# Kernel optimization log

Measured on AMD Instinct MI355X. Metric: run time of the kernel, lower is better.

Reference implementation:

```python
import jax, jax.numpy as jnp
import numpy as np

NUM_HEADS = 32
NUM_KV_HEADS = 8
HEAD_DIM = 64
HIDDEN = 2048
EPS = 1e-05
ROPE_THETA = 1000000.0


def _rmsnorm(x, w):
    # x: [..., head_dim]
    var = jnp.mean(x * x, axis=-1, keepdims=True)
    return w * (x * jax.lax.rsqrt(var + EPS))


def _rope(q, k):
    # q,k: [B, h, T, d]
    T, d = q.shape[2], q.shape[3]
    inv_freq = 1.0 / (ROPE_THETA ** (jnp.arange(0, d, 2, dtype=jnp.float32) / d))
    t = jnp.arange(T, dtype=jnp.float32)
    freqs = jnp.outer(t, inv_freq)               # [T, d/2]
    emb = jnp.concatenate([freqs, freqs], -1)    # [T, d]
    cos = jnp.cos(emb)[None, None].astype(q.dtype)
    sin = jnp.sin(emb)[None, None].astype(q.dtype)

    def rotate(x):
        x1, x2 = x[..., : d // 2], x[..., d // 2 :]
        return jnp.concatenate([-x2, x1], -1)

    return q * cos + rotate(q) * sin, k * cos + rotate(k) * sin


def setup_inputs() -> dict:
    key = jax.random.key(0)
    ks = jax.random.split(key, 7)
    s = 0.02
    x = jax.random.normal(ks[0], (2, 2048, HIDDEN), jnp.float32)
    Wq = jax.random.normal(ks[1], (HIDDEN, NUM_HEADS * HEAD_DIM), jnp.float32) * s
    Wk = jax.random.normal(ks[2], (HIDDEN, NUM_KV_HEADS * HEAD_DIM), jnp.float32) * s
    Wv = jax.random.normal(ks[3], (HIDDEN, NUM_KV_HEADS * HEAD_DIM), jnp.float32) * s
    Wo = jax.random.normal(ks[4], (NUM_HEADS * HEAD_DIM, HIDDEN), jnp.float32) * s
    q_ln_w = jnp.ones((HEAD_DIM,), jnp.float32)
    k_ln_w = jnp.ones((HEAD_DIM,), jnp.float32)
    return {"x": x, "Wq": Wq, "Wk": Wk, "Wv": Wv, "Wo": Wo, "q_ln_w": q_ln_w, "k_ln_w": k_ln_w}


def reference(x, Wq, Wk, Wv, Wo, q_ln_w, k_ln_w):
    B, T, _ = x.shape
    g = NUM_HEADS // NUM_KV_HEADS  # GQA groups = 4
    q = (x @ Wq).reshape(B, T, NUM_HEADS, HEAD_DIM)
    k = (x @ Wk).reshape(B, T, NUM_KV_HEADS, HEAD_DIM)
    v = (x @ Wv).reshape(B, T, NUM_KV_HEADS, HEAD_DIM)
    q = _rmsnorm(q, q_ln_w)
    k = _rmsnorm(k, k_ln_w)
    q = q.transpose(0, 2, 1, 3)  # [B, nh, T, d]
    k = k.transpose(0, 2, 1, 3)  # [B, nkv, T, d]
    v = v.transpose(0, 2, 1, 3)
    q, k = _rope(q, k)
    # native GQA: fold query heads into (kv_head, group) without repeating K/V
    qg = q.reshape(B, NUM_KV_HEADS, g, T, HEAD_DIM)
    scale = 1.0 / jnp.sqrt(jnp.array(HEAD_DIM, q.dtype))
    scores = jnp.einsum("bkgtd,bksd->bkgts", qg, k) * scale  # [B,nkv,g,T,T]
    causal = jnp.tril(jnp.ones((T, T), bool))
    scores = jnp.where(causal, scores, jnp.finfo(scores.dtype).min)
    probs = jax.nn.softmax(scores, axis=-1)
    out = jnp.einsum("bkgts,bksd->bkgtd", probs, v)  # [B,nkv,g,T,d]
    out = out.reshape(B, NUM_HEADS, T, HEAD_DIM).transpose(0, 2, 1, 3).reshape(B, T, -1)
    return out @ Wo
```

## Files before the change

kernel.cpp:

```cpp
#include <hip/hip_runtime.h>
#include <cstdint>
#include <cstddef>

typedef unsigned short u16;
typedef __attribute__((ext_vector_type(8))) short short8;
typedef __attribute__((ext_vector_type(4))) short short4v;
typedef __attribute__((ext_vector_type(4))) float float4v;
typedef __attribute__((ext_vector_type(4))) unsigned short ushort4v;
typedef __attribute__((ext_vector_type(2))) float float2v;

__device__ __forceinline__ u16 f2bf(float f) {
    union { float f; uint32_t u; } x; x.f = f;
    uint32_t r = x.u + 0x7fffu + ((x.u >> 16) & 1u);
    return (u16)(r >> 16);
}
__device__ __forceinline__ uint32_t pack_bf16x2(float lo, float hi) {
    union { float f; uint32_t u; } a, b; a.f = lo; b.f = hi;
    return __builtin_amdgcn_perm(b.u + 0x8000u, a.u + 0x8000u, 0x07060302u);
}
__device__ __forceinline__ void gl_lds16(const u16* g, u16* l) {
    __builtin_amdgcn_global_load_lds(
        (const __attribute__((address_space(1))) void*)g,
        (__attribute__((address_space(3))) void*)l, 16, 0, 0);
}

__global__ __launch_bounds__(256) void prep(const float4v* __restrict__ x,
                                            const float* __restrict__ Wq,
                                            const float* __restrict__ Wk,
                                            const float* __restrict__ Wv,
                                            const float* __restrict__ Wo,
                                            ushort4v* __restrict__ xb,
                                            u16* __restrict__ wqkv_t,
                                            u16* __restrict__ wo_t,
                                            float2v* __restrict__ tab) {
    __shared__ float lds[32][33];
    const int bid = blockIdx.x;
    const int tid = threadIdx.x;
    if (bid < 8192) {
        const int i = bid * 256 + tid;
        float4v v = x[i];
        ushort4v o;
        #pragma unroll
        for (int j = 0; j < 4; ++j) o[j] = f2bf(v[j]);
        xb[i] = o;
        return;
    }
    if (bid < 8448) {
        const int idx = (bid - 8192) * 256 + tid;
        const int t = idx >> 5;
        const int i = idx & 31;
        const float invf = exp2f(-(float)i * (19.931568569324174f / 32.0f));
        float sv, cv;
        sincosf((float)t * invf, &sv, &cv);
        float2v o; o[0] = cv; o[1] = sv;
        tab[idx] = o;
        return;
    }
    const float* src;
    int Ns, n0, k0, scol0;
    u16* dst;
    if (bid < 14592) {
        const int id = bid - 8448;
        const int bx = id % 96, by = id / 96;
        n0 = bx * 32; k0 = by * 32;
        if (n0 < 2048)      { src = Wq; Ns = 2048; scol0 = n0; }
        else if (n0 < 2560) { src = Wk; Ns = 512;  scol0 = n0 - 2048; }
        else                { src = Wv; Ns = 512;  scol0 = n0 - 2560; }
        dst = wqkv_t;
    } else {
        const int id = bid - 14592;
        const int bx = id & 63, by = id >> 6;
        n0 = bx * 32; k0 = by * 32;
        src = Wo; Ns = 2048; scol0 = n0;
        dst = wo_t;
    }
    const int row = tid >> 3;
    const int c4  = (tid & 7) * 4;
    const float4v v = *(const float4v*)(src + (size_t)(k0 + row) * Ns + scol0 + c4);
    #pragma unroll
    for (int i = 0; i < 4; ++i) lds[row][c4 + i] = v[i];
    __syncthreads();
    const int nrow = tid >> 3;
    const int k4   = (tid & 7) * 4;
    ushort4v o;
    #pragma unroll
    for (int i = 0; i < 4; ++i) o[i] = f2bf(lds[k4 + i][nrow]);
    *(ushort4v*)(dst + (size_t)(n0 + nrow) * 2048 + k0 + k4) = o;
}

__global__ __launch_bounds__(256, 3) void gemm_bt(const u16* __restrict__ A,
                                                  const u16* __restrict__ Bt,
                                                  float* __restrict__ C,
                                                  int M, int N, int K) {
    __shared__ u16 lds_a[128 * 32];
    __shared__ u16 lds_b[128 * 32];
    const int tid  = threadIdx.x;
    const int wave = tid >> 6;
    const int lane = tid & 63;
    const int quad = lane >> 4;
    const int l15  = lane & 15;
    const long m0 = (long)blockIdx.x * 128;
    const long n0 = (long)blockIdx.y * 128;
    const int wm = (wave >> 1) * 64;
    const int wn = (wave & 1) * 64;
    const int s_row = tid >> 2;
    const int s_col = (tid & 3) * 8;

    float4v acc[4][4];
    #pragma unroll
    for (int i = 0; i < 4; ++i)
        #pragma unroll
        for (int j = 0; j < 4; ++j)
            #pragma unroll
            for (int r = 0; r < 4; ++r) acc[i][j][r] = 0.0f;

    const u16* ga0 = A  + (m0 + s_row) * (long)K + s_col;
    const u16* ga1 = ga0 + 64 * (long)K;
    const u16* gb0 = Bt + (n0 + s_row) * (long)K + s_col;
    const u16* gb1 = gb0 + 64 * (long)K;
    u16* la = lds_a + tid * 8;
    u16* lb = lds_b + tid * 8;

    const int n_k = K >> 5;
    for (int it = 0; it < n_k; ++it) {
        const int k0 = it << 5;
        gl_lds16(ga0 + k0, la);
        gl_lds16(ga1 + k0, la + 2048);
        gl_lds16(gb0 + k0, lb);
        gl_lds16(gb1 + k0, lb + 2048);
        __syncthreads();
        short8 af[4], bfr[4];
        #pragma unroll
        for (int mt = 0; mt < 4; ++mt)
            af[mt] = *(const short8*)(lds_a + (wm + mt * 16 + l15) * 32 + quad * 8);
        #pragma unroll
        for (int nt = 0; nt < 4; ++nt)
            bfr[nt] = *(const short8*)(lds_b + (wn + nt * 16 + l15) * 32 + quad * 8);
        #pragma unroll
        for (int mt = 0; mt < 4; ++mt)
            #pragma unroll
            for (int nt = 0; nt < 4; ++nt)
                acc[mt][nt] = __builtin_amdgcn_mfma_f32_16x16x32_bf16(af[mt], bfr[nt], acc[mt][nt], 0, 0, 0);
        __syncthreads();
    }
    #pragma unroll
    for (int mt = 0; mt < 4; ++mt) {
        #pragma unroll
        for (int nt = 0; nt < 4; ++nt) {
            const long gr = m0 + wm + mt * 16 + quad * 4;
            const long gc = n0 + wn + nt * 16 + l15;
            #pragma unroll
            for (int r = 0; r < 4; ++r)
                C[(gr + r) * N + gc] = acc[mt][nt][r];
        }
    }
}

__global__ __launch_bounds__(256, 3) void gemm_qkv(const u16* __restrict__ A,
                                                   const u16* __restrict__ Bt,
                                                   const float* __restrict__ qw,
                                                   const float* __restrict__ kw,
                                                   const float2v* __restrict__ tab,
                                                   u16* __restrict__ Qr,
                                                   u16* __restrict__ Kr,
                                                   u16* __restrict__ Vt) {
    const int K = 2048;
    __shared__ u16 lds_a[128 * 32];
    __shared__ u16 lds_b[128 * 32];
    const int tid  = threadIdx.x;
    const int wave = tid >> 6;
    const int lane = tid & 63;
    const int quad = lane >> 4;
    const int l15  = lane & 15;
    const long m0 = (long)blockIdx.x * 128;
    const long n0 = (long)blockIdx.y * 128;
    const int wm = (wave >> 1) * 64;
    const int wn = (wave & 1) * 64;
    const int s_row = tid >> 2;
    const int s_col = (tid & 3) * 8;

    float4v acc[4][4];
    #pragma unroll
    for (int i = 0; i < 4; ++i)
        #pragma unroll
        for (int j = 0; j < 4; ++j)
            #pragma unroll
            for (int r = 0; r < 4; ++r) acc[i][j][r] = 0.0f;

    const u16* ga0 = A  + (m0 + s_row) * (long)K + s_col;
    const u16* ga1 = ga0 + 64 * (long)K;
    const u16* gb0 = Bt + (n0 + s_row) * (long)K + s_col;
    const u16* gb1 = gb0 + 64 * (long)K;
    u16* la = lds_a + tid * 8;
    u16* lb = lds_b + tid * 8;

    const int n_k = K >> 5;
    for (int it = 0; it < n_k; ++it) {
        const int k0 = it << 5;
        gl_lds16(ga0 + k0, la);
        gl_lds16(ga1 + k0, la + 2048);
        gl_lds16(gb0 + k0, lb);
        gl_lds16(gb1 + k0, lb + 2048);
        __syncthreads();
        short8 af[4], bfr[4];
        #pragma unroll
        for (int mt = 0; mt < 4; ++mt)
            af[mt] = *(const short8*)(lds_a + (wm + mt * 16 + l15) * 32 + quad * 8);
        #pragma unroll
        for (int nt = 0; nt < 4; ++nt)
            bfr[nt] = *(const short8*)(lds_b + (wn + nt * 16 + l15) * 32 + quad * 8);
        #pragma unroll
        for (int mt = 0; mt < 4; ++mt)
            #pragma unroll
            for (int nt = 0; nt < 4; ++nt)
                acc[mt][nt] = __builtin_amdgcn_mfma_f32_16x16x32_bf16(af[mt], bfr[nt], acc[mt][nt], 0, 0, 0);
        __syncthreads();
    }

    const int col0 = (int)n0 + wn;
    if (col0 < 2560) {
        const bool isQ = (col0 < 2048);
        const float* lw = isQ ? qw : kw;
        float wreg[4];
        #pragma unroll
        for (int nt = 0; nt < 4; ++nt) wreg[nt] = lw[nt * 16 + l15];
        const float qs = isQ ? 0.18033688011112042f : 1.0f;
        const int swm = isQ ? 0 : 7;
        u16* dst = isQ ? (Qr + ((size_t)(col0 >> 6)) * 2048 * 64)
                       : (Kr + ((size_t)((col0 - 2048) >> 6)) * 2048 * 64);
        const size_t head_stride = isQ ? ((size_t)32 * 2048 * 64) : ((size_t)8 * 2048 * 64);
        #pragma unroll
        for (int mt = 0; mt < 4; ++mt) {
            const int gr0 = (int)m0 + wm + mt * 16 + quad * 4;
            const int b = gr0 >> 11, tt0 = gr0 & 2047;
            float rms[4];
            #pragma unroll
            for (int r = 0; r < 4; ++r) {
                float s = 0.0f;
                #pragma unroll
                for (int nt = 0; nt < 4; ++nt) s += acc[mt][nt][r] * acc[mt][nt][r];
                s += __shfl_xor(s, 1);
                s += __shfl_xor(s, 2);
                s += __shfl_xor(s, 4);
                s += __shfl_xor(s, 8);
                rms[r] = rsqrtf(s * (1.0f / 64.0f) + 1e-5f);
            }
            u16* rowp = dst + (size_t)b * head_stride + (size_t)tt0 * 64;
            #pragma unroll
            for (int nt = 0; nt < 2; ++nt) {
                const int i = nt * 16 + l15;
                #pragma unroll
                for (int r = 0; r < 4; ++r) {
                    const float2v cs = tab[(tt0 + r) * 32 + i];
                    const float v1 = acc[mt][nt][r]     * rms[r] * wreg[nt];
                    const float v2 = acc[mt][nt + 2][r] * rms[r] * wreg[nt + 2];
                    const float o1 = (v1 * cs[0] - v2 * cs[1]) * qs;
                    const float o2 = (v2 * cs[0] + v1 * cs[1]) * qs;
                    const int k7 = (tt0 + r) & swm;
                    const int i1 = (((i >> 3) ^ k7) << 3) | (i & 7);
                    const int i2 = ((((i + 32) >> 3) ^ k7) << 3) | (i & 7);
                    rowp[(size_t)r * 64 + i1] = f2bf(o1);
                    rowp[(size_t)r * 64 + i2] = f2bf(o2);
                }
            }
        }
    } else {
        const int kh = (col0 - 2560) >> 6;
        #pragma unroll
        for (int mt = 0; mt < 4; ++mt) {
            const int gr0 = (int)m0 + wm + mt * 16 + quad * 4;
            const int b = gr0 >> 11, tt0 = gr0 & 2047;
            const int tb = tt0 & ~127;
            const int tl = tt0 & 127;
            const int p0b = ((tl & 15) >> 2) * 32 + (tl >> 4) * 4;
            #pragma unroll
            for (int nt = 0; nt < 4; ++nt) {
                const int d = nt * 16 + l15;
                ushort4v o;
                #pragma unroll
                for (int r = 0; r < 4; ++r) o[r] = f2bf(acc[mt][nt][r]);
                const int col = tb + ((((p0b >> 3) ^ (d & 7)) << 3) | (p0b & 7));
                *(ushort4v*)(Vt + (((size_t)(b * 8 + kh)) * 64 + d) * 2048 + col) = o;
            }
        }
    }
}

#define SOFTMAX_PACK(S, m_i, l_i, O, pf)                                    \
    {                                                                       \
        float mx = S[0][0];                                                 \
        _Pragma("unroll")                                                   \
        for (int nt = 0; nt < 8; ++nt)                                      \
            _Pragma("unroll")                                               \
            for (int r = 0; r < 4; ++r) mx = fmaxf(mx, S[nt][r]);           \
        mx = fmaxf(mx, __shfl_xor(mx, 16));                                 \
        mx = fmaxf(mx, __shfl_xor(mx, 32));                                 \
        const float mnew = fmaxf(m_i, mx);                                  \
        const float alpha = __builtin_amdgcn_exp2f(m_i - mnew);             \
        m_i = mnew;                                                         \
        float rs = 0.0f;                                                    \
        _Pragma("unroll")                                                   \
        for (int nt = 0; nt < 8; ++nt)                                      \
            _Pragma("unroll")                                               \
            for (int r = 0; r < 4; ++r) {                                   \
                const float pv = __builtin_amdgcn_exp2f(S[nt][r] - mnew);   \
                S[nt][r] = pv;                                              \
                rs += pv;                                                   \
            }                                                               \
        rs += __shfl_xor(rs, 16);                                           \
        rs += __shfl_xor(rs, 32);                                           \
        l_i = l_i * alpha + rs;                                             \
        _Pragma("unroll")                                                   \
        for (int dt = 0; dt < 4; ++dt)                                      \
            _Pragma("unroll")                                               \
            for (int r = 0; r < 4; ++r) O[dt][r] *= alpha;                  \
        _Pragma("unroll")                                                   \
        for (int nt = 0; nt < 8; ++nt) {                                    \
            union { uint32_t u[2]; short4v s; } pu;                         \
            pu.u[0] = pack_bf16x2(S[nt][0], S[nt][1]);                      \
            pu.u[1] = pack_bf16x2(S[nt][2], S[nt][3]);                      \
            pf[nt] = pu.s;                                                  \
        }                                                                   \
    }

#define WRITE_O(O, l_i, qrow)                                               \
    {                                                                       \
        const float rl = 1.0f / l_i;                                        \
        _Pragma("unroll")                                                   \
        for (int dt = 0; dt < 4; ++dt) {                                    \
            ushort4v o;                                                     \
            _Pragma("unroll")                                               \
            for (int r = 0; r < 4; ++r) o[r] = f2bf(O[dt][r] * rl);         \
            *(ushort4v*)(Ob + ((size_t)(b * 2048 + (qrow))) * 2048 +        \
                         h * 64 + dt * 16 + quad * 4) = o;                  \
        }                                                                   \
    }

__global__ __launch_bounds__(512, 2) void attn_fwd(const u16* __restrict__ Qr,
                                                   const u16* __restrict__ Kr,
                                                   const u16* __restrict__ Vt,
                                                   u16* __restrict__ Ob) {
    __shared__ u16 lds_k[2][128 * 64];
    __shared__ u16 lds_v[2][64 * 128];
    const int tid  = threadIdx.x;
    const int wave = tid >> 6;
    const int lane = tid & 63;
    const int quad = lane >> 4;
    const int l15  = lane & 15;
    const int sw7  = l15 & 7;
    const int qxB = blockIdx.y;
    const int qxA = 7 - qxB;
    const int bh = blockIdx.x;
    const int b = bh >> 5, h = bh & 31;
    const int kh = h >> 2;
    const u16* Qh = Qr + ((size_t)(b * 32 + h))  * 2048 * 64;
    const u16* Kh = Kr + ((size_t)(b * 8 + kh))  * 2048 * 64;
    const u16* Vh = Vt + ((size_t)(b * 8 + kh))  * 64 * 2048;

    const int w32 = wave * 32;
    int qrow_c0 = qxA * 256 + w32 + l15;
    int qrow_c1 = qrow_c0 + 16;
    short8 qf[2][2];
    #pragma unroll
    for (int ks = 0; ks < 2; ++ks) {
        qf[0][ks] = *(const short8*)(Qh + (size_t)qrow_c0 * 64 + ks * 32 + quad * 8);
        qf[1][ks] = *(const short8*)(Qh + (size_t)qrow_c1 * 64 + ks * 32 + quad * 8);
    }

    float m0v = -3e38f, l0v = 0.0f, m1v = -3e38f, l1v = 0.0f;
    float4v O0[4], O1[4];
    #pragma unroll
    for (int dt = 0; dt < 4; ++dt)
        #pragma unroll
        for (int r = 0; r < 4; ++r) { O0[dt][r] = 0.0f; O1[dt][r] = 0.0f; }

    const int vrow = tid >> 4;
    const int vchk = (tid & 15) * 8;
    auto stage = [&](int pb, int k0) {
        #pragma unroll
        for (int j = 0; j < 2; ++j)
            gl_lds16(Kh + (size_t)k0 * 64 + (j * 512 + tid) * 8,
                     &lds_k[pb][(j * 512 + tid) * 8]);
        #pragma unroll
        for (int j = 0; j < 2; ++j)
            gl_lds16(Vh + (size_t)(j * 32 + vrow) * 2048 + k0 + vchk,
                     &lds_v[pb][(j * 512 + tid) * 8]);
    };
    stage(0, 0);
    __syncthreads();

    const int nA = 2 * qxA + 2;
    const int n_it = 18;
    for (int i = 0; i < n_it; ++i) {
        const int p = i & 1;
        const int kt_cur = (i < nA) ? i : (i - nA);
        const int kt0 = kt_cur << 7;

        if (i + 1 < n_it) {
            const int ip1 = i + 1;
            const int ktn = (ip1 < nA) ? ip1 : (ip1 - nA);
            stage(1 - p, ktn << 7);
        }

        float4v S0[8], S1[8];
        #pragma unroll
        for (int nt = 0; nt < 8; ++nt)
            #pragma unroll
            for (int r = 0; r < 4; ++r) { S0[nt][r] = 0.0f; S1[nt][r] = 0.0f; }
        __builtin_amdgcn_s_setprio(1);
        #pragma unroll
        for (int ks = 0; ks < 2; ++ks) {
            #pragma unroll
            for (int nt = 0; nt < 8; ++nt) {
                short8 kf = *(const short8*)(lds_k[p] + (nt * 16 + l15) * 64 +
                                             (((ks * 4 + quad) ^ sw7) << 3));
                S0[nt] = __builtin_amdgcn_mfma_f32_16x16x32_bf16(kf, qf[0][ks], S0[nt], 0, 0, 0);
                S1[nt] = __builtin_amdgcn_mfma_f32_16x16x32_bf16(kf, qf[1][ks], S1[nt], 0, 0, 0);
            }
        }
        __builtin_amdgcn_s_setprio(0);

        if ((i >= nA - 2 && i < nA) || (i >= n_it - 2)) {
            #pragma unroll
            for (int nt = 0; nt < 8; ++nt) {
                const int keyb = kt0 + nt * 16 + quad * 4;
                #pragma unroll
                for (int r = 0; r < 4; ++r) {
                    if (keyb + r > qrow_c0) S0[nt][r] = -3e38f;
                    if (keyb + r > qrow_c1) S1[nt][r] = -3e38f;
                }
            }
        }

        short4v pf0[8], pf1[8];
        SOFTMAX_PACK(S0, m0v, l0v, O0, pf0);
        SOFTMAX_PACK(S1, m1v, l1v, O1, pf1);

        __builtin_amdgcn_s_setprio(1);
        #pragma unroll
        for (int nt2 = 0; nt2 < 4; ++nt2) {
            #pragma unroll
            for (int dt = 0; dt < 4; ++dt) {
                short8 vv = *(const short8*)(lds_v[p] + (dt * 16 + l15) * 128 +
                                             (((quad * 4 + nt2) ^ sw7) << 3));
                short4v vlo = __builtin_shufflevector(vv, vv, 0, 1, 2, 3);
                short4v vhi = __builtin_shufflevector(vv, vv, 4, 5, 6, 7);
                O0[dt] = __builtin_amdgcn_mfma_f32_16x16x16bf16_1k(vlo, pf0[2 * nt2],     O0[dt], 0, 0, 0);
                O0[dt] = __builtin_amdgcn_mfma_f32_16x16x16bf16_1k(vhi, pf0[2 * nt2 + 1], O0[dt], 0, 0, 0);
                O1[dt] = __builtin_amdgcn_mfma_f32_16x16x16bf16_1k(vlo, pf1[2 * nt2],     O1[dt], 0, 0, 0);
                O1[dt] = __builtin_amdgcn_mfma_f32_16x16x16bf16_1k(vhi, pf1[2 * nt2 + 1], O1[dt], 0, 0, 0);
            }
        }
        __builtin_amdgcn_s_setprio(0);

        if (i == nA - 1) {
            WRITE_O(O0, l0v, qrow_c0);
            WRITE_O(O1, l1v, qrow_c1);
            m0v = -3e38f; l0v = 0.0f; m1v = -3e38f; l1v = 0.0f;
            #pragma unroll
            for (int dt = 0; dt < 4; ++dt)
                #pragma unroll
                for (int r = 0; r < 4; ++r) { O0[dt][r] = 0.0f; O1[dt][r] = 0.0f; }
            qrow_c0 = qxB * 256 + w32 + l15;
            qrow_c1 = qrow_c0 + 16;
            #pragma unroll
            for (int ks = 0; ks < 2; ++ks) {
                qf[0][ks] = *(const short8*)(Qh + (size_t)qrow_c0 * 64 + ks * 32 + quad * 8);
                qf[1][ks] = *(const short8*)(Qh + (size_t)qrow_c1 * 64 + ks * 32 + quad * 8);
            }
        }
        __syncthreads();
    }
    WRITE_O(O0, l0v, qrow_c0);
    WRITE_O(O1, l1v, qrow_c1);
}

extern "C" void kernel_launch(void* const* d_in, const int* in_sizes, int n_in,
                              void* d_out, int out_size, void* d_ws, size_t ws_size,
                              hipStream_t stream) {
    (void)in_sizes; (void)n_in; (void)out_size; (void)ws_size;
    const float* x  = (const float*)d_in[0];
    const float* Wq = (const float*)d_in[1];
    const float* Wk = (const float*)d_in[2];
    const float* Wv = (const float*)d_in[3];
    const float* Wo = (const float*)d_in[4];
    const float* qw = (const float*)d_in[5];
    const float* kw = (const float*)d_in[6];
    float* out = (float*)d_out;

    char* ws = (char*)d_ws;
    size_t off = 0;
    auto alloc = [&](size_t bytes) {
        char* p = ws + off;
        off += (bytes + 255) & ~(size_t)255;
        return p;
    };
    u16* xb     = (u16*)alloc((size_t)8388608 * 2);
    u16* wqkv_t = (u16*)alloc((size_t)3072 * 2048 * 2);
    u16* wo_t   = (u16*)alloc((size_t)2048 * 2048 * 2);
    u16* q_r    = (u16*)alloc((size_t)2 * 32 * 2048 * 64 * 2);
    u16* k_r    = (u16*)alloc((size_t)2 * 8 * 2048 * 64 * 2);
    u16* v_r    = (u16*)alloc((size_t)2 * 8 * 64 * 2048 * 2);
    float2v* rtab = (float2v*)alloc((size_t)2048 * 32 * 8);
    u16* attnb  = xb;

    hipLaunchKernelGGL(prep, dim3(18688), dim3(256), 0, stream,
                       (const float4v*)x, Wq, Wk, Wv, Wo,
                       (ushort4v*)xb, wqkv_t, wo_t, rtab);
    hipLaunchKernelGGL(gemm_qkv, dim3(32, 24), dim3(256), 0, stream,
                       xb, wqkv_t, qw, kw, rtab, q_r, k_r, v_r);
    hipLaunchKernelGGL(attn_fwd, dim3(64, 4), dim3(512), 0, stream, q_r, k_r, v_r, attnb);
    hipLaunchKernelGGL(gemm_bt, dim3(32, 16), dim3(256), 0, stream,
                       attnb, wo_t, out, 4096, 2048, 2048);
}
```

Before: 291.4 us.

## Restructure attention to 128-row query blocks with 64-key tiles, dropping paired scheduling

The attention kernel moves from 512-thread blocks, which each handled two paired 256-row query chunks (a long one and a short one for causal balance) over 128-key tiles, to 256-thread blocks that each handle one 128-row query chunk over 64-key tiles. The grid grows to 16 query blocks per head, with the longest chunks launched first. The V transpose layout in the QKV GEMM epilogue switches to 64-column swizzle blocks to match the smaller tile. This cuts LDS use and raises occupancy, in exchange for more K/V reloads per head and more barrier iterations, and it relies on hardware scheduling rather than explicit pairing to balance the causal work.

```diff
diff --git a/kernel.cpp b/kernel.cpp
--- a/kernel.cpp
+++ b/kernel.cpp
@@ -270,9 +270,9 @@
         for (int mt = 0; mt < 4; ++mt) {
             const int gr0 = (int)m0 + wm + mt * 16 + quad * 4;
             const int b = gr0 >> 11, tt0 = gr0 & 2047;
-            const int tb = tt0 & ~127;
-            const int tl = tt0 & 127;
-            const int p0b = ((tl & 15) >> 2) * 32 + (tl >> 4) * 4;
+            const int tb = tt0 & ~63;
+            const int tl = tt0 & 63;
+            const int p0b = ((tl & 15) >> 2) * 16 + (tl >> 4) * 4;
             #pragma unroll
             for (int nt = 0; nt < 4; ++nt) {
                 const int d = nt * 16 + l15;
@@ -290,7 +290,7 @@
     {                                                                       \
         float mx = S[0][0];                                                 \
         _Pragma("unroll")                                                   \
-        for (int nt = 0; nt < 8; ++nt)                                      \
+        for (int nt = 0; nt < 4; ++nt)                                      \
             _Pragma("unroll")                                               \
             for (int r = 0; r < 4; ++r) mx = fmaxf(mx, S[nt][r]);           \
         mx = fmaxf(mx, __shfl_xor(mx, 16));                                 \
@@ -300,7 +300,7 @@
         m_i = mnew;                                                         \
         float rs = 0.0f;                                                    \
         _Pragma("unroll")                                                   \
-        for (int nt = 0; nt < 8; ++nt)                                      \
+        for (int nt = 0; nt < 4; ++nt)                                      \
             _Pragma("unroll")                                               \
             for (int r = 0; r < 4; ++r) {                                   \
                 const float pv = __builtin_amdgcn_exp2f(S[nt][r] - mnew);   \
@@ -315,7 +315,7 @@
             _Pragma("unroll")                                               \
             for (int r = 0; r < 4; ++r) O[dt][r] *= alpha;                  \
         _Pragma("unroll")                                                   \
-        for (int nt = 0; nt < 8; ++nt) {                                    \
+        for (int nt = 0; nt < 4; ++nt) {                                    \
             union { uint32_t u[2]; short4v s; } pu;                         \
             pu.u[0] = pack_bf16x2(S[nt][0], S[nt][1]);                      \
             pu.u[1] = pack_bf16x2(S[nt][2], S[nt][3]);                      \
@@ -336,20 +336,19 @@
         }                                                                   \
     }
 
-__global__ __launch_bounds__(512, 2) void attn_fwd(const u16* __restrict__ Qr,
+__global__ __launch_bounds__(256, 4) void attn_fwd(const u16* __restrict__ Qr,
                                                    const u16* __restrict__ Kr,
                                                    const u16* __restrict__ Vt,
                                                    u16* __restrict__ Ob) {
-    __shared__ u16 lds_k[2][128 * 64];
-    __shared__ u16 lds_v[2][64 * 128];
+    __shared__ u16 lds_k[2][64 * 64];
+    __shared__ u16 lds_v[2][64 * 64];
     const int tid  = threadIdx.x;
     const int wave = tid >> 6;
     const int lane = tid & 63;
     const int quad = lane >> 4;
     const int l15  = lane & 15;
     const int sw7  = l15 & 7;
-    const int qxB = blockIdx.y;
-    const int qxA = 7 - qxB;
+    const int qx = 15 - blockIdx.y;
     const int bh = blockIdx.x;
     const int b = bh >> 5, h = bh & 31;
     const int kh = h >> 2;
@@ -357,9 +356,8 @@
     const u16* Kh = Kr + ((size_t)(b * 8 + kh))  * 2048 * 64;
     const u16* Vh = Vt + ((size_t)(b * 8 + kh))  * 64 * 2048;
 
-    const int w32 = wave * 32;
-    int qrow_c0 = qxA * 256 + w32 + l15;
-    int qrow_c1 = qrow_c0 + 16;
+    const int qrow_c0 = qx * 128 + wave * 32 + l15;
+    const int qrow_c1 = qrow_c0 + 16;
     short8 qf[2][2];
     #pragma unroll
     for (int ks = 0; ks < 2; ++ks) {
@@ -374,44 +372,38 @@
         #pragma unroll
         for (int r = 0; r < 4; ++r) { O0[dt][r] = 0.0f; O1[dt][r] = 0.0f; }
 
-    const int vrow = tid >> 4;
-    const int vchk = (tid & 15) * 8;
+    const int vrow = tid >> 3;
+    const int vchk = (tid & 7) * 8;
     auto stage = [&](int pb, int k0) {
         #pragma unroll
         for (int j = 0; j < 2; ++j)
-            gl_lds16(Kh + (size_t)k0 * 64 + (j * 512 + tid) * 8,
-                     &lds_k[pb][(j * 512 + tid) * 8]);
+            gl_lds16(Kh + (size_t)k0 * 64 + (j * 256 + tid) * 8,
+                     &lds_k[pb][(j * 256 + tid) * 8]);
         #pragma unroll
         for (int j = 0; j < 2; ++j)
             gl_lds16(Vh + (size_t)(j * 32 + vrow) * 2048 + k0 + vchk,
-                     &lds_v[pb][(j * 512 + tid) * 8]);
+                     &lds_v[pb][(j * 256 + tid) * 8]);
     };
     stage(0, 0);
     __syncthreads();
 
-    const int nA = 2 * qxA + 2;
-    const int n_it = 18;
+    const int n_it = 2 * qx + 2;
     for (int i = 0; i < n_it; ++i) {
         const int p = i & 1;
-        const int kt_cur = (i < nA) ? i : (i - nA);
-        const int kt0 = kt_cur << 7;
-
-        if (i + 1 < n_it) {
-            const int ip1 = i + 1;
-            const int ktn = (ip1 < nA) ? ip1 : (ip1 - nA);
-            stage(1 - p, ktn << 7);
-        }
-
-        float4v S0[8], S1[8];
-        #pragma unroll
-        for (int nt = 0; nt < 8; ++nt)
+        const int kt0 = i << 6;
+
+        if (i + 1 < n_it) stage(1 - p, (i + 1) << 6);
+
+        float4v S0[4], S1[4];
+        #pragma unroll
+        for (int nt = 0; nt < 4; ++nt)
             #pragma unroll
             for (int r = 0; r < 4; ++r) { S0[nt][r] = 0.0f; S1[nt][r] = 0.0f; }
         __builtin_amdgcn_s_setprio(1);
         #pragma unroll
         for (int ks = 0; ks < 2; ++ks) {
             #pragma unroll
-            for (int nt = 0; nt < 8; ++nt) {
+            for (int nt = 0; nt < 4; ++nt) {
                 short8 kf = *(const short8*)(lds_k[p] + (nt * 16 + l15) * 64 +
                                              (((ks * 4 + quad) ^ sw7) << 3));
                 S0[nt] = __builtin_amdgcn_mfma_f32_16x16x32_bf16(kf, qf[0][ks], S0[nt], 0, 0, 0);
@@ -420,9 +412,9 @@
         }
         __builtin_amdgcn_s_setprio(0);
 
-        if ((i >= nA - 2 && i < nA) || (i >= n_it - 2)) {
-            #pragma unroll
-            for (int nt = 0; nt < 8; ++nt) {
+        if (i >= n_it - 2) {
+            #pragma unroll
+            for (int nt = 0; nt < 4; ++nt) {
                 const int keyb = kt0 + nt * 16 + quad * 4;
                 #pragma unroll
                 for (int r = 0; r < 4; ++r) {
@@ -432,17 +424,17 @@
             }
         }
 
-        short4v pf0[8], pf1[8];
+        short4v pf0[4], pf1[4];
         SOFTMAX_PACK(S0, m0v, l0v, O0, pf0);
         SOFTMAX_PACK(S1, m1v, l1v, O1, pf1);
 
         __builtin_amdgcn_s_setprio(1);
         #pragma unroll
-        for (int nt2 = 0; nt2 < 4; ++nt2) {
+        for (int nt2 = 0; nt2 < 2; ++nt2) {
             #pragma unroll
             for (int dt = 0; dt < 4; ++dt) {
-                short8 vv = *(const short8*)(lds_v[p] + (dt * 16 + l15) * 128 +
-                                             (((quad * 4 + nt2) ^ sw7) << 3));
+                short8 vv = *(const short8*)(lds_v[p] + (dt * 16 + l15) * 64 +
+                                             (((quad * 2 + nt2) ^ sw7) << 3));
                 short4v vlo = __builtin_shufflevector(vv, vv, 0, 1, 2, 3);
                 short4v vhi = __builtin_shufflevector(vv, vv, 4, 5, 6, 7);
                 O0[dt] = __builtin_amdgcn_mfma_f32_16x16x16bf16_1k(vlo, pf0[2 * nt2],     O0[dt], 0, 0, 0);
@@ -453,22 +445,6 @@
         }
         __builtin_amdgcn_s_setprio(0);
 
-        if (i == nA - 1) {
-            WRITE_O(O0, l0v, qrow_c0);
-            WRITE_O(O1, l1v, qrow_c1);
-            m0v = -3e38f; l0v = 0.0f; m1v = -3e38f; l1v = 0.0f;
-            #pragma unroll
-            for (int dt = 0; dt < 4; ++dt)
-                #pragma unroll
-                for (int r = 0; r < 4; ++r) { O0[dt][r] = 0.0f; O1[dt][r] = 0.0f; }
-            qrow_c0 = qxB * 256 + w32 + l15;
-            qrow_c1 = qrow_c0 + 16;
-            #pragma unroll
-            for (int ks = 0; ks < 2; ++ks) {
-                qf[0][ks] = *(const short8*)(Qh + (size_t)qrow_c0 * 64 + ks * 32 + quad * 8);
-                qf[1][ks] = *(const short8*)(Qh + (size_t)qrow_c1 * 64 + ks * 32 + quad * 8);
-            }
-        }
         __syncthreads();
     }
     WRITE_O(O0, l0v, qrow_c0);
@@ -509,7 +485,7 @@
                        (ushort4v*)xb, wqkv_t, wo_t, rtab);
     hipLaunchKernelGGL(gemm_qkv, dim3(32, 24), dim3(256), 0, stream,
                        xb, wqkv_t, qw, kw, rtab, q_r, k_r, v_r);
-    hipLaunchKernelGGL(attn_fwd, dim3(64, 4), dim3(512), 0, stream, q_r, k_r, v_r, attnb);
+    hipLaunchKernelGGL(attn_fwd, dim3(64, 16), dim3(256), 0, stream, q_r, k_r, v_r, attnb);
     hipLaunchKernelGGL(gemm_bt, dim3(32, 16), dim3(256), 0, stream,
                        attnb, wo_t, out, 4096, 2048, 2048);
 }
```

New measurement: 288.1 us. Within noise of the previous version (-1.1%).
